# Kernel optimization log

Hardware: AMD Instinct MI355X
Metric: run time of the kernel (lower is better)

## Reference

```python
import jax, jax.numpy as jnp
import numpy as np

D_MODEL, D_FF, H, B, S = 1024, 4096, 16, 4, 2048
D_K = D_MODEL // H
EPS = 1e-5
NEG = -1e9


def _custom_ln(x, alpha, bias):
    # torch: mean, std (unbiased, N-1), alpha*(x-mean)/(std+eps)+bias; alpha/bias scalars
    mean = jnp.mean(x, axis=-1, keepdims=True)
    n = x.shape[-1]
    var = jnp.sum((x - mean) ** 2, axis=-1, keepdims=True) / (n - 1)
    std = jnp.sqrt(var)
    return alpha * (x - mean) / (std + EPS) + bias


def setup_inputs() -> dict:
    key = jax.random.key(0)
    ks = jax.random.split(key, 12)
    sc_d = 1.0 / np.sqrt(D_MODEL)
    sc_f = 1.0 / np.sqrt(D_FF)
    inp = {
        "x": jax.random.normal(ks[0], (B, S, D_MODEL), jnp.float32),
        "src_mask": jnp.ones((B, 1, 1, S), jnp.int32),
        "wq": jax.random.normal(ks[1], (D_MODEL, D_MODEL), jnp.float32) * sc_d,
        "bq": jnp.zeros((D_MODEL,), jnp.float32),
        "wk": jax.random.normal(ks[2], (D_MODEL, D_MODEL), jnp.float32) * sc_d,
        "bk": jnp.zeros((D_MODEL,), jnp.float32),
        "wv": jax.random.normal(ks[3], (D_MODEL, D_MODEL), jnp.float32) * sc_d,
        "bv": jnp.zeros((D_MODEL,), jnp.float32),
        "wo": jax.random.normal(ks[4], (D_MODEL, D_MODEL), jnp.float32) * sc_d,
        "bo": jnp.zeros((D_MODEL,), jnp.float32),
        "w1": jax.random.normal(ks[5], (D_MODEL, D_FF), jnp.float32) * sc_d,
        "b1": jnp.zeros((D_FF,), jnp.float32),
        "w2": jax.random.normal(ks[6], (D_FF, D_MODEL), jnp.float32) * sc_f,
        "b2": jnp.zeros((D_MODEL,), jnp.float32),
        "ln1_a": jnp.ones((1,), jnp.float32),
        "ln1_b": jnp.zeros((1,), jnp.float32),
        "ln2_a": jnp.ones((1,), jnp.float32),
        "ln2_b": jnp.zeros((1,), jnp.float32),
    }
    return inp


def _attention(xn, src_mask, wq, bq, wk, bk, wv, bv, wo, bo):
    q = (xn @ wq + bq).reshape(B, S, H, D_K).transpose(0, 2, 1, 3)  # [B,H,S,Dk]
    k = (xn @ wk + bk).reshape(B, S, H, D_K).transpose(0, 2, 1, 3)
    v = (xn @ wv + bv).reshape(B, S, H, D_K).transpose(0, 2, 1, 3)
    scores = jnp.einsum("bhqd,bhkd->bhqk", q, k) / np.sqrt(D_K)
    scores = jnp.where(src_mask == 0, NEG, scores)
    attn = jax.nn.softmax(scores, axis=-1)
    ctx = jnp.einsum("bhqk,bhkd->bhqd", attn, v)
    ctx = ctx.transpose(0, 2, 1, 3).reshape(B, S, D_MODEL)
    return ctx @ wo + bo


def reference(x, src_mask, wq, bq, wk, bk, wv, bv, wo, bo,
              w1, b1, w2, b2, ln1_a, ln1_b, ln2_a, ln2_b):
    # pre-LN attention residual (dropout=0 -> identity)
    xn = _custom_ln(x, ln1_a, ln1_b)
    x = x + _attention(xn, src_mask, wq, bq, wk, bk, wv, bv, wo, bo)
    # pre-LN FFN residual
    xn = _custom_ln(x, ln2_a, ln2_b)
    ff = jax.nn.relu(xn @ w1 + b1) @ w2 + b2
    return x + ff
```

## Files before the change

kernel.cpp:

```cpp
#include <hip/hip_runtime.h>

typedef unsigned short u16;
typedef __bf16 bf16x8 __attribute__((ext_vector_type(8)));
typedef float f32x4 __attribute__((ext_vector_type(4)));

__device__ __forceinline__ u16 f2bf(float f) {
  unsigned u = __builtin_bit_cast(unsigned, f);
  unsigned lsb = (u >> 16) & 1u;
  u += 0x7fffu + lsb;
  return (u16)(u >> 16);
}

__device__ __forceinline__ float bf2f(u16 b) {
  return __builtin_bit_cast(float, (unsigned)b << 16);
}

__device__ __forceinline__ unsigned cvt_pk_bf16(float lo, float hi) {
  unsigned r;
  asm("v_cvt_pk_bf16_f32 %0, %1, %2" : "=v"(r) : "v"(lo), "v"(hi));
  return r;
}

__device__ __forceinline__ void gld_lds16(const u16* g, u16* l) {
  __builtin_amdgcn_global_load_lds(
      (__attribute__((address_space(1))) void*)g,
      (__attribute__((address_space(3))) void*)l, 16, 0, 0);
}

__global__ __launch_bounds__(256) void ln_kernel(
    const float* __restrict__ x, u16* __restrict__ out,
    const float* __restrict__ alpha_p, const float* __restrict__ beta_p) {
  const int row = blockIdx.x;
  const int t = threadIdx.x;
  const float4 v = reinterpret_cast<const float4*>(x + (size_t)row * 1024)[t];
  float s = v.x + v.y + v.z + v.w;
  float sq = v.x * v.x + v.y * v.y + v.z * v.z + v.w * v.w;
#pragma unroll
  for (int off = 32; off > 0; off >>= 1) {
    s += __shfl_down(s, off);
    sq += __shfl_down(sq, off);
  }
  __shared__ float red[8];
  const int w = t >> 6;
  if ((t & 63) == 0) { red[w] = s; red[4 + w] = sq; }
  __syncthreads();
  const float ts = red[0] + red[1] + red[2] + red[3];
  const float tq = red[4] + red[5] + red[6] + red[7];
  const float mean = ts * (1.0f / 1024.0f);
  float var = (tq - ts * mean) * (1.0f / 1023.0f);
  var = fmaxf(var, 0.0f);
  const float rden = 1.0f / (sqrtf(var) + 1e-5f);
  const float a = alpha_p[0], bb = beta_p[0];
  uint2 ov;
  ov.x = cvt_pk_bf16(a * (v.x - mean) * rden + bb, a * (v.y - mean) * rden + bb);
  ov.y = cvt_pk_bf16(a * (v.z - mean) * rden + bb, a * (v.w - mean) * rden + bb);
  reinterpret_cast<uint2*>(out + (size_t)row * 1024)[t] = ov;
}

__global__ __launch_bounds__(256) void ln_kernel_bf(
    const u16* __restrict__ x, u16* __restrict__ out,
    const float* __restrict__ alpha_p, const float* __restrict__ beta_p) {
  const int row = blockIdx.x;
  const int t = threadIdx.x;
  const uint2 raw = reinterpret_cast<const uint2*>(x + (size_t)row * 1024)[t];
  float v0 = bf2f((u16)(raw.x & 0xffff)), v1 = bf2f((u16)(raw.x >> 16));
  float v2 = bf2f((u16)(raw.y & 0xffff)), v3 = bf2f((u16)(raw.y >> 16));
  float s = v0 + v1 + v2 + v3;
  float sq = v0 * v0 + v1 * v1 + v2 * v2 + v3 * v3;
#pragma unroll
  for (int off = 32; off > 0; off >>= 1) {
    s += __shfl_down(s, off);
    sq += __shfl_down(sq, off);
  }
  __shared__ float red[8];
  const int w = t >> 6;
  if ((t & 63) == 0) { red[w] = s; red[4 + w] = sq; }
  __syncthreads();
  const float ts = red[0] + red[1] + red[2] + red[3];
  const float tq = red[4] + red[5] + red[6] + red[7];
  const float mean = ts * (1.0f / 1024.0f);
  float var = (tq - ts * mean) * (1.0f / 1023.0f);
  var = fmaxf(var, 0.0f);
  const float rden = 1.0f / (sqrtf(var) + 1e-5f);
  const float a = alpha_p[0], bb = beta_p[0];
  uint2 ov;
  ov.x = cvt_pk_bf16(a * (v0 - mean) * rden + bb, a * (v1 - mean) * rden + bb);
  ov.y = cvt_pk_bf16(a * (v2 - mean) * rden + bb, a * (v3 - mean) * rden + bb);
  reinterpret_cast<uint2*>(out + (size_t)row * 1024)[t] = ov;
}

__global__ __launch_bounds__(256) void wcvt_t(
    const float* __restrict__ w, u16* __restrict__ wt, int K, int N, float scale) {
  __shared__ float tile[32][33];
  const int n0 = blockIdx.x * 32, k0 = blockIdx.y * 32;
  const int tx = threadIdx.x, ty = threadIdx.y;
#pragma unroll
  for (int i = 0; i < 4; ++i)
    tile[ty + i * 8][tx] = w[(size_t)(k0 + ty + i * 8) * N + n0 + tx];
  __syncthreads();
#pragma unroll
  for (int i = 0; i < 4; ++i)
    wt[(size_t)(n0 + ty + i * 8) * K + k0 + tx] = f2bf(tile[tx][ty + i * 8] * scale);
}

__global__ __launch_bounds__(256) void wcvt_t4(
    const float* __restrict__ w0, const float* __restrict__ w1,
    const float* __restrict__ w2, const float* __restrict__ w3,
    u16* __restrict__ dqkv, u16* __restrict__ dwo, float qscale) {
  __shared__ float tile[32][33];
  const int z = blockIdx.z;
  const float* w = (z == 0) ? w0 : (z == 1) ? w1 : (z == 2) ? w2 : w3;
  u16* wt = (z < 3) ? (dqkv + (size_t)z * 1024 * 1024) : dwo;
  const float scale = (z == 0) ? qscale : 1.f;
  const int n0 = blockIdx.x * 32, k0 = blockIdx.y * 32;
  const int tx = threadIdx.x, ty = threadIdx.y;
#pragma unroll
  for (int i = 0; i < 4; ++i)
    tile[ty + i * 8][tx] = w[(size_t)(k0 + ty + i * 8) * 1024 + n0 + tx];
  __syncthreads();
#pragma unroll
  for (int i = 0; i < 4; ++i)
    wt[(size_t)(n0 + ty + i * 8) * 1024 + k0 + tx] = f2bf(tile[tx][ty + i * 8] * scale);
}

__global__ __launch_bounds__(256) void pack_bias(
    const float* __restrict__ a, const float* __restrict__ b,
    const float* __restrict__ c, float* __restrict__ o, float qscale) {
  const int i = blockIdx.x * 256 + threadIdx.x;
  o[i] = (i < 1024) ? a[i] * qscale : ((i < 2048) ? b[i - 1024] : c[i - 2048]);
}

__global__ __launch_bounds__(256) void mk_mbias(
    const int* __restrict__ mask, float* __restrict__ mb, int* __restrict__ flags) {
  const int b = blockIdx.x, t = threadIdx.x;
  __shared__ int bad;
  if (t == 0) bad = 0;
  __syncthreads();
  int loc = 0;
#pragma unroll
  for (int i = 0; i < 8; ++i) {
    const int idx = b * 2048 + t * 8 + i;
    const int mv = mask[idx];
    mb[idx] = mv ? 0.f : -1.4427e9f;
    loc |= (mv == 0);
  }
  if (loc) atomicOr(&bad, 1);
  __syncthreads();
  if (t == 0) flags[b] = !bad;
}

template <int EPI, int DEPTH>
__global__ __launch_bounds__(512, 4) void gemm8(
    const u16* __restrict__ A, const u16* __restrict__ Bt,
    const float* __restrict__ bias, const void* __restrict__ res,
    void* __restrict__ Cout, u16* __restrict__ vt, int M, int N, int K) {
  constexpr int BM = 128, BN = 256;
  constexpr int VMC = 3;
  constexpr int PD = DEPTH - 1;
  constexpr int MF = 4;
  extern __shared__ u16 smem[];
  u16* Asb = smem;
  u16* Bsb = smem + DEPTH * BM * 32;

  const int tid = threadIdx.x;
  const int l = tid & 63;
  const int w = tid >> 6;
  const int wr = w >> 2, wc = w & 3;
  const int gx = gridDim.x;
  int id = blockIdx.y * gx + blockIdx.x;
  const int nwg = gx * gridDim.y;
  id = (id & 7) * (nwg >> 3) + (id >> 3);
  const int n0 = (id % gx) * BN;
  const int m0 = (id / gx) * BM;
  const int lr = l & 15, lg = l >> 4;
  const int koff = (lg ^ ((lr >> 1) & 3)) * 8;

  f32x4 acc[MF][4];
#pragma unroll
  for (int i = 0; i < MF; ++i)
#pragma unroll
    for (int j = 0; j < 4; ++j) acc[i][j] = f32x4{0.f, 0.f, 0.f, 0.f};

  const u16* aSrc;
  int aOff;
  {
    const int ci = tid;
    const int row = ci >> 2, c = ci & 3;
    const int sc = c ^ ((row >> 1) & 3);
    aSrc = A + (size_t)(m0 + row) * K + sc * 8;
    aOff = ci * 8;
  }
  const u16* bSrc[2];
  int bOff[2];
#pragma unroll
  for (int i = 0; i < 2; ++i) {
    const int ci = tid + i * 512;
    const int row = ci >> 2, c = ci & 3;
    const int sc = c ^ ((row >> 1) & 3);
    bSrc[i] = Bt + (size_t)(n0 + row) * K + sc * 8;
    bOff[i] = ci * 8;
  }

  const int NT = K >> 5;
#pragma unroll
  for (int s = 0; s < PD; ++s) {
    gld_lds16(aSrc + s * 32, Asb + s * BM * 32 + aOff);
#pragma unroll
    for (int i = 0; i < 2; ++i) gld_lds16(bSrc[i] + s * 32, Bsb + s * BN * 32 + bOff[i]);
  }
  if constexpr ((PD - 1) * VMC == 3) asm volatile("s_waitcnt vmcnt(3)" ::: "memory");
  else asm volatile("s_waitcnt vmcnt(6)" ::: "memory");
  __builtin_amdgcn_s_barrier();

  int cur = 0;
  for (int t = 0; t < NT; ++t) {
    if (t + PD < NT) {
      int nx = cur + PD;
      if (nx >= DEPTH) nx -= DEPTH;
      const int ko = (t + PD) * 32;
      gld_lds16(aSrc + ko, Asb + nx * BM * 32 + aOff);
#pragma unroll
      for (int i = 0; i < 2; ++i) gld_lds16(bSrc[i] + ko, Bsb + nx * BN * 32 + bOff[i]);
    }
    const u16* Ab = Asb + cur * BM * 32;
    const u16* Bb = Bsb + cur * BN * 32;
    bf16x8 a[MF], b[4];
#pragma unroll
    for (int mf = 0; mf < MF; ++mf)
      a[mf] = *reinterpret_cast<const bf16x8*>(&Ab[(wr * (BM / 2) + mf * 16 + lr) * 32 + koff]);
#pragma unroll
    for (int nf = 0; nf < 4; ++nf)
      b[nf] = *reinterpret_cast<const bf16x8*>(&Bb[(wc * 64 + nf * 16 + lr) * 32 + koff]);
    __builtin_amdgcn_s_setprio(1);
#pragma unroll
    for (int mf = 0; mf < MF; ++mf)
#pragma unroll
      for (int nf = 0; nf < 4; ++nf)
        acc[mf][nf] = __builtin_amdgcn_mfma_f32_16x16x32_bf16(a[mf], b[nf], acc[mf][nf], 0, 0, 0);
    __builtin_amdgcn_s_setprio(0);
    {
      const int ahead = NT - 2 - t;
      if constexpr (PD == 2) {
        if (ahead >= 1) asm volatile("s_waitcnt vmcnt(3)" ::: "memory");
        else asm volatile("s_waitcnt vmcnt(0)" ::: "memory");
      } else {
        if (ahead >= 2) asm volatile("s_waitcnt vmcnt(6)" ::: "memory");
        else if (ahead == 1) asm volatile("s_waitcnt vmcnt(3)" ::: "memory");
        else asm volatile("s_waitcnt vmcnt(0)" ::: "memory");
      }
    }
    __builtin_amdgcn_s_barrier();
    cur = (cur + 1 >= DEPTH) ? 0 : cur + 1;
  }

  if (EPI == 3 && n0 >= 2048) {
#pragma unroll
    for (int mf = 0; mf < MF; ++mf) {
#pragma unroll
      for (int nf = 0; nf < 4; ++nf) {
        const int col = n0 + wc * 64 + nf * 16 + lr;
        const float bv = bias[col];
        const int row0 = m0 + wr * (BM / 2) + mf * 16 + lg * 4;
        const int bb = row0 >> 11, s0 = row0 & 2047;
        const int d = col - 2048;
        uint2 pv;
        pv.x = cvt_pk_bf16(acc[mf][nf][0] + bv, acc[mf][nf][1] + bv);
        pv.y = cvt_pk_bf16(acc[mf][nf][2] + bv, acc[mf][nf][3] + bv);
        *reinterpret_cast<uint2*>(vt + ((size_t)bb * 1024 + d) * 2048 + s0) = pv;
      }
    }
    return;
  }

#pragma unroll
  for (int mf = 0; mf < MF; ++mf) {
#pragma unroll
    for (int nf = 0; nf < 4; ++nf) {
      const int col = n0 + wc * 64 + nf * 16 + lr;
      const float bv = bias[col];
#pragma unroll
      for (int j = 0; j < 4; ++j) {
        const int row = m0 + wr * (BM / 2) + mf * 16 + lg * 4 + j;
        const size_t idx = (size_t)row * N + col;
        const float vv = acc[mf][nf][j] + bv;
        if (EPI == 4)
          ((u16*)Cout)[idx] = f2bf(vv + ((const float*)res)[idx]);
        else if (EPI == 5)
          ((float*)Cout)[idx] = vv + bf2f(((const u16*)res)[idx]);
        else if (EPI == 2)
          ((u16*)Cout)[idx] = f2bf(fmaxf(vv, 0.f));
        else
          ((u16*)Cout)[idx] = f2bf(vv);
      }
    }
  }
}

__global__ __launch_bounds__(512, 4) void attn_fwd9(
    const u16* __restrict__ qkv, const u16* __restrict__ vt,
    const float* __restrict__ mbias, const int* __restrict__ flags,
    u16* __restrict__ ctx) {
  __shared__ u16 Ks[2][64 * 64];
  __shared__ u16 Vs[2][64 * 64];
  const int tid = threadIdx.x;
  const int l = tid & 63;
  const int w = tid >> 6;
  const int p = blockIdx.y * 8 + blockIdx.x;
  const int idx = p >> 3;
  const int bh = (p & 7) * 8 + (idx >> 3);
  const int qx = idx & 7;
  const int b = bh >> 4, h = bh & 15;
  const int r0 = qx * 256 + w * 32;
  const int lr = l & 15, lg = l >> 4;

  const u16* qb = qkv + (size_t)b * 2048 * 3072 + h * 64;
  const u16* kp = qb + 1024;
  const u16* vb = vt + ((size_t)b * 1024 + h * 64) * 2048;
  const float* mb = mbias + (size_t)b * 2048;
  const int allLive = flags[b];

  bf16x8 qf[2][2];
#pragma unroll
  for (int m = 0; m < 2; ++m)
#pragma unroll
    for (int ks = 0; ks < 2; ++ks)
      qf[m][ks] = *reinterpret_cast<const bf16x8*>(
          qb + (size_t)(r0 + m * 16 + lr) * 3072 + ks * 32 + lg * 8);

  bf16x8 ones;
#pragma unroll
  for (int e = 0; e < 8; ++e) ones[e] = (__bf16)1.0f;

  float mrun[2] = {-1e30f, -1e30f};
  f32x4 osum[2];
  f32x4 o[2][4];
#pragma unroll
  for (int m = 0; m < 2; ++m) {
    osum[m] = f32x4{0.f, 0.f, 0.f, 0.f};
#pragma unroll
    for (int d = 0; d < 4; ++d) o[m][d] = f32x4{0.f, 0.f, 0.f, 0.f};
  }

  const int srow = tid >> 3, scc = tid & 7;
  const int ssc = scc ^ (srow & 7);
  const u16* kS = kp + (size_t)srow * 3072 + ssc * 8;
  const u16* vS = vb + (size_t)srow * 2048 + ssc * 8;
  gld_lds16(kS, &Ks[0][tid * 8]);
  gld_lds16(vS, &Vs[0][tid * 8]);
  asm volatile("s_waitcnt vmcnt(0)" ::: "memory");
  __syncthreads();

  union U8 { unsigned u[4]; bf16x8 v; };

  int cur = 0;
  for (int t = 0; t < 32; ++t) {
    const int kb0 = t * 64;
    if (t + 1 < 32) {
      const int nb = kb0 + 64;
      gld_lds16(kS + (size_t)nb * 3072, &Ks[cur ^ 1][tid * 8]);
      gld_lds16(vS + nb, &Vs[cur ^ 1][tid * 8]);
    }

    f32x4 st[2][4];
    __builtin_amdgcn_s_setprio(1);
#pragma unroll
    for (int cf = 0; cf < 4; ++cf) {
      const int krow = cf * 16 + lr;
      const int ch0 = lg ^ (krow & 7);
      const int ch1 = (4 + lg) ^ (krow & 7);
      const bf16x8 kf0 = *reinterpret_cast<const bf16x8*>(&Ks[cur][krow * 64 + ch0 * 8]);
      const bf16x8 kf1 = *reinterpret_cast<const bf16x8*>(&Ks[cur][krow * 64 + ch1 * 8]);
#pragma unroll
      for (int m = 0; m < 2; ++m) {
        f32x4 acc = __builtin_amdgcn_mfma_f32_16x16x32_bf16(kf0, qf[m][0],
                                                            f32x4{0.f, 0.f, 0.f, 0.f}, 0, 0, 0);
        st[m][cf] = __builtin_amdgcn_mfma_f32_16x16x32_bf16(kf1, qf[m][1], acc, 0, 0, 0);
      }
    }
    __builtin_amdgcn_s_setprio(0);

    if (!allLive) {
#pragma unroll
      for (int cf = 0; cf < 4; ++cf) {
        const float4 m4 = *reinterpret_cast<const float4*>(mb + kb0 + cf * 16 + lg * 4);
#pragma unroll
        for (int m = 0; m < 2; ++m) {
          st[m][cf][0] += m4.x;
          st[m][cf][1] += m4.y;
          st[m][cf][2] += m4.z;
          st[m][cf][3] += m4.w;
        }
      }
    }

    bf16x8 paA[2], paB[2];
#pragma unroll
    for (int m = 0; m < 2; ++m) {
      float p0 = fmaxf(fmaxf(st[m][0][0], st[m][0][1]), st[m][0][2]);
      float p1 = fmaxf(fmaxf(st[m][0][3], st[m][1][0]), st[m][1][1]);
      float p2 = fmaxf(fmaxf(st[m][1][2], st[m][1][3]), st[m][2][0]);
      float p3 = fmaxf(fmaxf(st[m][2][1], st[m][2][2]), st[m][2][3]);
      float p4 = fmaxf(fmaxf(st[m][3][0], st[m][3][1]), st[m][3][2]);
      float pm = fmaxf(fmaxf(p0, p1), p2);
      pm = fmaxf(fmaxf(pm, p3), p4);
      pm = fmaxf(pm, st[m][3][3]);
      pm = fmaxf(pm, __shfl_xor(pm, 16));
      pm = fmaxf(pm, __shfl_xor(pm, 32));
      if (__any(pm > mrun[m] + 8.f)) {
        const float mn = fmaxf(mrun[m], pm);
        const float corr = exp2f(mrun[m] - mn);
        mrun[m] = mn;
#pragma unroll
        for (int j = 0; j < 4; ++j) osum[m][j] *= corr;
#pragma unroll
        for (int d = 0; d < 4; ++d)
#pragma unroll
          for (int j = 0; j < 4; ++j) o[m][d][j] *= corr;
      }
#pragma unroll
      for (int cf = 0; cf < 4; ++cf)
#pragma unroll
        for (int j = 0; j < 4; ++j)
          st[m][cf][j] = exp2f(st[m][cf][j] - mrun[m]);

      unsigned pk[4][2];
#pragma unroll
      for (int cf = 0; cf < 4; ++cf)
#pragma unroll
        for (int wp = 0; wp < 2; ++wp)
          pk[cf][wp] = cvt_pk_bf16(st[m][cf][2 * wp], st[m][cf][2 * wp + 1]);

      U8 a0, a1;
#pragma unroll
      for (int c = 0; c < 2; ++c) {
        const int src = lr + 16 * ((2 * lg + c) & 3);
#pragma unroll
        for (int wp = 0; wp < 2; ++wp) {
          const int v00 = __shfl((int)pk[0][wp], src);
          const int v01 = __shfl((int)pk[1][wp], src);
          const int v10 = __shfl((int)pk[2][wp], src);
          const int v11 = __shfl((int)pk[3][wp], src);
          a0.u[2 * c + wp] = (unsigned)((lg < 2) ? v00 : v01);
          a1.u[2 * c + wp] = (unsigned)((lg < 2) ? v10 : v11);
        }
      }
      paA[m] = a0.v;
      paB[m] = a1.v;
    }

    __builtin_amdgcn_s_setprio(1);
#pragma unroll
    for (int df = 0; df < 4; ++df) {
      const int vrow = df * 16 + lr;
      const int ch0 = lg ^ (vrow & 7);
      const int ch1 = (4 + lg) ^ (vrow & 7);
      const bf16x8 vf0 = *reinterpret_cast<const bf16x8*>(&Vs[cur][vrow * 64 + ch0 * 8]);
      const bf16x8 vf1 = *reinterpret_cast<const bf16x8*>(&Vs[cur][vrow * 64 + ch1 * 8]);
#pragma unroll
      for (int m = 0; m < 2; ++m) {
        o[m][df] = __builtin_amdgcn_mfma_f32_16x16x32_bf16(vf0, paA[m], o[m][df], 0, 0, 0);
        o[m][df] = __builtin_amdgcn_mfma_f32_16x16x32_bf16(vf1, paB[m], o[m][df], 0, 0, 0);
      }
    }
#pragma unroll
    for (int m = 0; m < 2; ++m) {
      osum[m] = __builtin_amdgcn_mfma_f32_16x16x32_bf16(ones, paA[m], osum[m], 0, 0, 0);
      osum[m] = __builtin_amdgcn_mfma_f32_16x16x32_bf16(ones, paB[m], osum[m], 0, 0, 0);
    }
    __builtin_amdgcn_s_setprio(0);

    asm volatile("s_waitcnt vmcnt(0)" ::: "memory");
    __syncthreads();
    cur ^= 1;
  }

#pragma unroll
  for (int m = 0; m < 2; ++m) {
    const float rdiv = 1.f / osum[m][0];
    const size_t rowbase = ((size_t)b * 2048 + r0 + m * 16 + lr) * 1024 + h * 64;
#pragma unroll
    for (int df = 0; df < 4; ++df) {
      uint2 s4;
      s4.x = cvt_pk_bf16(o[m][df][0] * rdiv, o[m][df][1] * rdiv);
      s4.y = cvt_pk_bf16(o[m][df][2] * rdiv, o[m][df][3] * rdiv);
      *reinterpret_cast<uint2*>(ctx + rowbase + df * 16 + lg * 4) = s4;
    }
  }
}

extern "C" void kernel_launch(void* const* d_in, const int* in_sizes, int n_in,
                              void* d_out, int out_size, void* d_ws, size_t ws_size,
                              hipStream_t stream) {
  const float* x = (const float*)d_in[0];
  const int* mask = (const int*)d_in[1];
  const float* wq = (const float*)d_in[2];
  const float* bq = (const float*)d_in[3];
  const float* wk = (const float*)d_in[4];
  const float* bk = (const float*)d_in[5];
  const float* wv = (const float*)d_in[6];
  const float* bv = (const float*)d_in[7];
  const float* wo = (const float*)d_in[8];
  const float* bo = (const float*)d_in[9];
  const float* w1 = (const float*)d_in[10];
  const float* b1 = (const float*)d_in[11];
  const float* w2 = (const float*)d_in[12];
  const float* b2 = (const float*)d_in[13];
  const float* ln1a = (const float*)d_in[14];
  const float* ln1b = (const float*)d_in[15];
  const float* ln2a = (const float*)d_in[16];
  const float* ln2b = (const float*)d_in[17];

  const float SCL2 = 0.125f * 1.4426950408889634f;
  const size_t LDS128_3 = 3 * (128 + 256) * 32 * sizeof(u16);
  const size_t LDS128_4 = 4 * (128 + 256) * 32 * sizeof(u16);

  (void)hipFuncSetAttribute((const void*)&gemm8<3, 3>,
                            hipFuncAttributeMaxDynamicSharedMemorySize, (int)LDS128_3);
  (void)hipFuncSetAttribute((const void*)&gemm8<2, 3>,
                            hipFuncAttributeMaxDynamicSharedMemorySize, (int)LDS128_3);
  (void)hipFuncSetAttribute((const void*)&gemm8<4, 4>,
                            hipFuncAttributeMaxDynamicSharedMemorySize, (int)LDS128_4);
  (void)hipFuncSetAttribute((const void*)&gemm8<5, 4>,
                            hipFuncAttributeMaxDynamicSharedMemorySize, (int)LDS128_4);

  char* ws = (char*)d_ws;
  const size_t MB = 1024ull * 1024ull;
  u16* WTQKV = (u16*)(ws + 0 * MB);
  u16* WTO = (u16*)(ws + 6 * MB);
  u16* W1T = (u16*)(ws + 8 * MB);
  u16* W2T = (u16*)(ws + 16 * MB);
  float* BQKV = (float*)(ws + 24 * MB);
  float* MBIAS = (float*)(ws + 24 * MB + 65536);
  int* FLAGS = (int*)(ws + 24 * MB + 131072);
  u16* QKV = (u16*)(ws + 25 * MB);
  u16* VT = (u16*)(ws + 73 * MB);
  u16* XN = (u16*)(ws + 89 * MB);
  u16* CTX = (u16*)(ws + 105 * MB);
  u16* X2 = (u16*)(ws + 25 * MB);
  u16* XN2 = (u16*)(ws + 57 * MB);
  u16* H1 = (u16*)(ws + 73 * MB);

  dim3 bt(32, 8);
  wcvt_t4<<<dim3(32, 32, 4), bt, 0, stream>>>(wq, wk, wv, wo, WTQKV, WTO, SCL2);
  wcvt_t<<<dim3(128, 32), bt, 0, stream>>>(w1, W1T, 1024, 4096, 1.f);
  wcvt_t<<<dim3(32, 128), bt, 0, stream>>>(w2, W2T, 4096, 1024, 1.f);
  pack_bias<<<dim3(12), 256, 0, stream>>>(bq, bk, bv, BQKV, SCL2);
  mk_mbias<<<dim3(4), 256, 0, stream>>>(mask, MBIAS, FLAGS);

  ln_kernel<<<8192, 256, 0, stream>>>(x, XN, ln1a, ln1b);
  gemm8<3, 3><<<dim3(12, 64), 512, LDS128_3, stream>>>(XN, WTQKV, BQKV, nullptr, QKV, VT, 8192, 3072, 1024);
  attn_fwd9<<<dim3(8, 64), 512, 0, stream>>>(QKV, VT, MBIAS, FLAGS, CTX);
  gemm8<4, 4><<<dim3(4, 64), 512, LDS128_4, stream>>>(CTX, WTO, bo, x, X2, nullptr, 8192, 1024, 1024);
  ln_kernel_bf<<<8192, 256, 0, stream>>>(X2, XN2, ln2a, ln2b);
  gemm8<2, 3><<<dim3(16, 64), 512, LDS128_3, stream>>>(XN2, W1T, b1, nullptr, H1, nullptr, 8192, 4096, 1024);
  gemm8<5, 4><<<dim3(4, 64), 512, LDS128_4, stream>>>(H1, W2T, b2, X2, (float*)d_out, nullptr, 8192, 1024, 4096);
}
```

Baseline: 427.9 us.

## Split attention over the key dimension and merge partial results

The attention kernel now splits the key/value sequence into two halves on a third grid dimension. Each half writes unnormalized fp32 partial outputs plus its running max and row sum, and a new merge kernel rescales and combines them into the bf16 context. This doubles the number of attention blocks to raise occupancy or parallelism on the device. The cost is extra fp32 traffic, roughly 64MB of partials written and read back, plus an additional kernel launch. The output buffer is reused as scratch for one partial.

```diff
diff --git a/kernel.cpp b/kernel.cpp
--- a/kernel.cpp
+++ b/kernel.cpp
@@ -296,15 +296,17 @@
   }
 }
 
-__global__ __launch_bounds__(512, 4) void attn_fwd9(
+__global__ __launch_bounds__(512, 4) void attn_fwd11(
     const u16* __restrict__ qkv, const u16* __restrict__ vt,
     const float* __restrict__ mbias, const int* __restrict__ flags,
-    u16* __restrict__ ctx) {
+    float* __restrict__ op0, float* __restrict__ op1,
+    float2* __restrict__ mst) {
   __shared__ u16 Ks[2][64 * 64];
   __shared__ u16 Vs[2][64 * 64];
   const int tid = threadIdx.x;
   const int l = tid & 63;
   const int w = tid >> 6;
+  const int sp = blockIdx.z;
   const int p = blockIdx.y * 8 + blockIdx.x;
   const int idx = p >> 3;
   const int bh = (p & 7) * 8 + (idx >> 3);
@@ -312,11 +314,12 @@
   const int b = bh >> 4, h = bh & 15;
   const int r0 = qx * 256 + w * 32;
   const int lr = l & 15, lg = l >> 4;
+  float* __restrict__ op = sp ? op1 : op0;
 
   const u16* qb = qkv + (size_t)b * 2048 * 3072 + h * 64;
   const u16* kp = qb + 1024;
   const u16* vb = vt + ((size_t)b * 1024 + h * 64) * 2048;
-  const float* mb = mbias + (size_t)b * 2048;
+  const float* mb = mbias + (size_t)b * 2048 + sp * 1024;
   const int allLive = flags[b];
 
   bf16x8 qf[2][2];
@@ -343,8 +346,8 @@
 
   const int srow = tid >> 3, scc = tid & 7;
   const int ssc = scc ^ (srow & 7);
-  const u16* kS = kp + (size_t)srow * 3072 + ssc * 8;
-  const u16* vS = vb + (size_t)srow * 2048 + ssc * 8;
+  const u16* kS = kp + (size_t)(sp * 1024 + srow) * 3072 + ssc * 8;
+  const u16* vS = vb + (size_t)srow * 2048 + sp * 1024 + ssc * 8;
   gld_lds16(kS, &Ks[0][tid * 8]);
   gld_lds16(vS, &Vs[0][tid * 8]);
   asm volatile("s_waitcnt vmcnt(0)" ::: "memory");
@@ -353,9 +356,9 @@
   union U8 { unsigned u[4]; bf16x8 v; };
 
   int cur = 0;
-  for (int t = 0; t < 32; ++t) {
+  for (int t = 0; t < 16; ++t) {
     const int kb0 = t * 64;
-    if (t + 1 < 32) {
+    if (t + 1 < 16) {
       const int nb = kb0 + 64;
       gld_lds16(kS + (size_t)nb * 3072, &Ks[cur ^ 1][tid * 8]);
       gld_lds16(vS + nb, &Vs[cur ^ 1][tid * 8]);
@@ -476,16 +479,41 @@
 
 #pragma unroll
   for (int m = 0; m < 2; ++m) {
-    const float rdiv = 1.f / osum[m][0];
-    const size_t rowbase = ((size_t)b * 2048 + r0 + m * 16 + lr) * 1024 + h * 64;
+    const int grow = b * 2048 + r0 + m * 16 + lr;
+    if (lg == 0)
+      mst[((size_t)sp * 8192 + grow) * 16 + h] = float2{mrun[m], osum[m][0]};
+    const size_t rowbase = (size_t)grow * 1024 + h * 64;
 #pragma unroll
     for (int df = 0; df < 4; ++df) {
-      uint2 s4;
-      s4.x = cvt_pk_bf16(o[m][df][0] * rdiv, o[m][df][1] * rdiv);
-      s4.y = cvt_pk_bf16(o[m][df][2] * rdiv, o[m][df][3] * rdiv);
-      *reinterpret_cast<uint2*>(ctx + rowbase + df * 16 + lg * 4) = s4;
-    }
-  }
+      float4 s4;
+      s4.x = o[m][df][0];
+      s4.y = o[m][df][1];
+      s4.z = o[m][df][2];
+      s4.w = o[m][df][3];
+      *reinterpret_cast<float4*>(op + rowbase + df * 16 + lg * 4) = s4;
+    }
+  }
+}
+
+__global__ __launch_bounds__(256) void attn_merge(
+    const float* __restrict__ op0, const float* __restrict__ op1,
+    const float2* __restrict__ mst, u16* __restrict__ ctx) {
+  const int row = blockIdx.x;
+  const int t = threadIdx.x;
+  const int col = t * 4;
+  const int h = col >> 6;
+  const float2 s0 = mst[(size_t)row * 16 + h];
+  const float2 s1 = mst[(size_t)(8192 + row) * 16 + h];
+  const float M = fmaxf(s0.x, s1.x);
+  const float w0 = exp2f(s0.x - M);
+  const float w1 = exp2f(s1.x - M);
+  const float den = 1.f / (s0.y * w0 + s1.y * w1);
+  const float4 o0 = reinterpret_cast<const float4*>(op0 + (size_t)row * 1024)[t];
+  const float4 o1 = reinterpret_cast<const float4*>(op1 + (size_t)row * 1024)[t];
+  uint2 ov;
+  ov.x = cvt_pk_bf16((o0.x * w0 + o1.x * w1) * den, (o0.y * w0 + o1.y * w1) * den);
+  ov.y = cvt_pk_bf16((o0.z * w0 + o1.z * w1) * den, (o0.w * w0 + o1.w * w1) * den);
+  reinterpret_cast<uint2*>(ctx + (size_t)row * 1024)[t] = ov;
 }
 
 extern "C" void kernel_launch(void* const* d_in, const int* in_sizes, int n_in,
@@ -535,10 +563,13 @@
   u16* QKV = (u16*)(ws + 25 * MB);
   u16* VT = (u16*)(ws + 73 * MB);
   u16* XN = (u16*)(ws + 89 * MB);
-  u16* CTX = (u16*)(ws + 105 * MB);
+  u16* CTX = (u16*)(ws + 89 * MB);
+  float* OP1 = (float*)(ws + 105 * MB);
+  float2* MST = (float2*)(ws + 137 * MB);
   u16* X2 = (u16*)(ws + 25 * MB);
   u16* XN2 = (u16*)(ws + 57 * MB);
   u16* H1 = (u16*)(ws + 73 * MB);
+  float* OP0 = (float*)d_out;
 
   dim3 bt(32, 8);
   wcvt_t4<<<dim3(32, 32, 4), bt, 0, stream>>>(wq, wk, wv, wo, WTQKV, WTO, SCL2);
@@ -549,7 +580,8 @@
 
   ln_kernel<<<8192, 256, 0, stream>>>(x, XN, ln1a, ln1b);
   gemm8<3, 3><<<dim3(12, 64), 512, LDS128_3, stream>>>(XN, WTQKV, BQKV, nullptr, QKV, VT, 8192, 3072, 1024);
-  attn_fwd9<<<dim3(8, 64), 512, 0, stream>>>(QKV, VT, MBIAS, FLAGS, CTX);
+  attn_fwd11<<<dim3(8, 64, 2), 512, 0, stream>>>(QKV, VT, MBIAS, FLAGS, OP0, OP1, MST);
+  attn_merge<<<8192, 256, 0, stream>>>(OP0, OP1, MST, CTX);
   gemm8<4, 4><<<dim3(4, 64), 512, LDS128_4, stream>>>(CTX, WTO, bo, x, X2, nullptr, 8192, 1024, 1024);
   ln_kernel_bf<<<8192, 256, 0, stream>>>(X2, XN2, ln2a, ln2b);
   gemm8<2, 3><<<dim3(16, 64), 512, LDS128_3, stream>>>(XN2, W1T, b1, nullptr, H1, nullptr, 8192, 4096, 1024);
```

After: 440.8 us. +3.0%, slower.
